# Performance work log

Hardware: AMD Instinct MI355X
Metric: run time of the kernel (lower is better)

The kernel has to match this reference:

```python
import jax, jax.numpy as jnp
import numpy as np

B, N, C = 4, 2048, 768
H = 12
HD = C // H
SCALE = HD ** -0.5


def setup_inputs() -> dict:
    key = jax.random.key(0)
    k1, k2, k3 = jax.random.split(key, 3)
    x = jax.random.normal(k1, (B, N, C), dtype=jnp.float32)
    w_qkv = jax.random.normal(k2, (3 * C, C), dtype=jnp.float32) * (C ** -0.5)
    w_proj = jax.random.normal(k3, (C, C), dtype=jnp.float32) * (C ** -0.5)
    b_proj = jnp.zeros((C,), dtype=jnp.float32)
    return {"x": x, "w_qkv": w_qkv, "w_proj": w_proj, "b_proj": b_proj}


def reference(x, w_qkv, w_proj, b_proj):
    Bx, Nx, Cx = x.shape
    # qkv linear: x @ W^T -> [B, N, 3C], then split into heads
    qkv = jnp.einsum('bnc,dc->bnd', x, w_qkv)
    qkv = qkv.reshape(Bx, Nx, 3, H, HD).transpose(2, 0, 3, 1, 4)  # [3, B, H, N, HD]
    q, k, v = qkv[0], qkv[1], qkv[2]
    attn = jnp.einsum('bhqd,bhkd->bhqk', q, k) * SCALE  # [B, H, N, N]
    attn = jax.nn.softmax(attn, axis=-1)
    out = jnp.einsum('bhqk,bhkd->bhqd', attn, v)  # [B, H, N, HD]
    out = out.transpose(0, 2, 1, 3).reshape(Bx, Nx, Cx)
    out = jnp.einsum('bnc,dc->bnd', out, w_proj) + b_proj
    return out
```

## Files before the change

### kernel.cpp

```cpp
#include <hip/hip_runtime.h>
#include <hip/hip_bf16.h>
#include <stdint.h>

#define DI __device__ __forceinline__

typedef __bf16 bf16x8 __attribute__((ext_vector_type(8)));
typedef float f32x4 __attribute__((ext_vector_type(4)));
typedef unsigned short u16;

DI u16 f2bf(float f) {
  union { float f; uint32_t u; } x; x.f = f;
  uint32_t r = (x.u + 0x7FFFu + ((x.u >> 16) & 1u)) >> 16;
  return (u16)r;
}
DI bf16x8 load16(const u16* p) { return *(const bf16x8*)p; }

DI void async_copy16(void* lds, const void* g) {
  __builtin_amdgcn_global_load_lds(
      (const __attribute__((address_space(1))) uint32_t*)g,
      (__attribute__((address_space(3))) uint32_t*)lds, 16, 0, 0);
}

DI f32x4 mfma16(bf16x8 a, bf16x8 b, f32x4 c) {
  return __builtin_amdgcn_mfma_f32_16x16x32_bf16(a, b, c, 0, 0, 0);
}

DI uint32_t pk_bf16(float a, float b) {
  union { __hip_bfloat162 v; uint32_t u; } r;
  r.v = __float22bfloat162_rn(make_float2(a, b));
  return r.u;
}

#define QSCALE (0.125f * 1.44269504088896340736f)

__global__ __launch_bounds__(256)
void cvt_all(const float* __restrict__ s0, u16* __restrict__ d0, int n0,
             const float* __restrict__ s1, u16* __restrict__ d1, int n1,
             const float* __restrict__ s2, u16* __restrict__ d2, int n2) {
  int i = (blockIdx.x * 256 + threadIdx.x) * 4;
  const float* s; u16* d;
  if (i < n0) { s = s0 + i; d = d0 + i; }
  else if (i < n0 + n1) { s = s1 + (i - n0); d = d1 + (i - n0); }
  else if (i < n0 + n1 + n2) { s = s2 + (i - n0 - n1); d = d2 + (i - n0 - n1); }
  else return;
  float4 v = *(const float4*)s;
  ushort4 o;
  o.x = f2bf(v.x); o.y = f2bf(v.y); o.z = f2bf(v.z); o.w = f2bf(v.w);
  *(ushort4*)d = o;
}

__global__ __launch_bounds__(256)
void gemm_qkv(const u16* __restrict__ A, const u16* __restrict__ Bm,
              u16* __restrict__ Qb, u16* __restrict__ Kb, u16* __restrict__ Vt,
              int M, int N, int K) {
  __shared__ u16 As[128 * 32];
  __shared__ u16 Bs[128 * 32];

  const int tid  = threadIdx.x;
  const int lane = tid & 63;
  const int wave = tid >> 6;
  const int m0 = blockIdx.y * 128;
  const int n0 = blockIdx.x * 128;
  const int wm = (wave & 1) * 64;
  const int wn = (wave >> 1) * 64;
  const int c = lane & 15;
  const int g = lane >> 4;

  f32x4 acc[4][4] = {};

  for (int k0 = 0; k0 < K; k0 += 32) {
#pragma unroll
    for (int i = 0; i < 2; ++i) {
      int j = i * 256 + tid;
      int row = j >> 2;
      int col = (j & 3) * 8;
      async_copy16(&As[j * 8], &A[(size_t)(m0 + row) * K + k0 + col]);
      async_copy16(&Bs[j * 8], &Bm[(size_t)(n0 + row) * K + k0 + col]);
    }
    __syncthreads();

    bf16x8 af[4], bfr[4];
#pragma unroll
    for (int t = 0; t < 4; ++t) {
      af[t]  = *(const bf16x8*)&As[(wm + t * 16 + c) * 32 + g * 8];
      bfr[t] = *(const bf16x8*)&Bs[(wn + t * 16 + c) * 32 + g * 8];
    }
#pragma unroll
    for (int mt = 0; mt < 4; ++mt)
#pragma unroll
      for (int nt = 0; nt < 4; ++nt)
        acc[mt][nt] = mfma16(af[mt], bfr[nt], acc[mt][nt]);
    __syncthreads();
  }

  if (n0 < 768) {
#pragma unroll
    for (int nt = 0; nt < 4; ++nt) {
      int col = n0 + wn + nt * 16 + c;
#pragma unroll
      for (int mt = 0; mt < 4; ++mt)
#pragma unroll
        for (int r = 0; r < 4; ++r) {
          int row = m0 + wm + mt * 16 + g * 4 + r;
          Qb[(size_t)row * 768 + col] = f2bf(acc[mt][nt][r] * QSCALE);
        }
    }
  } else if (n0 < 1536) {
#pragma unroll
    for (int nt = 0; nt < 4; ++nt) {
      int col = n0 - 768 + wn + nt * 16 + c;
#pragma unroll
      for (int mt = 0; mt < 4; ++mt)
#pragma unroll
        for (int r = 0; r < 4; ++r) {
          int row = m0 + wm + mt * 16 + g * 4 + r;
          Kb[(size_t)row * 768 + col] = f2bf(acc[mt][nt][r]);
        }
    }
  } else {
#pragma unroll
    for (int nt = 0; nt < 4; ++nt) {
      int cv = n0 - 1536 + wn + nt * 16 + c;
      int hv = cv >> 6, d = cv & 63;
#pragma unroll
      for (int mt = 0; mt < 4; ++mt) {
        int row = m0 + wm + mt * 16 + g * 4;
        int b = row >> 11, nn = row & 2047;
        ushort4 o;
        o.x = f2bf(acc[mt][nt][0]); o.y = f2bf(acc[mt][nt][1]);
        o.z = f2bf(acc[mt][nt][2]); o.w = f2bf(acc[mt][nt][3]);
        *(ushort4*)&Vt[(((size_t)b * 12 + hv) * 64 + d) * 2048 + nn] = o;
      }
    }
  }
}

__global__ __launch_bounds__(256)
void gemm_proj(const u16* __restrict__ A, const u16* __restrict__ Bm,
               const float* __restrict__ bias, float* __restrict__ Co,
               int M, int N, int K) {
  __shared__ u16 As[128 * 32];
  __shared__ u16 Bs[128 * 32];

  const int tid  = threadIdx.x;
  const int lane = tid & 63;
  const int wave = tid >> 6;
  const int m0 = blockIdx.y * 128;
  const int n0 = blockIdx.x * 128;
  const int wm = (wave & 1) * 64;
  const int wn = (wave >> 1) * 64;
  const int c = lane & 15;
  const int g = lane >> 4;

  f32x4 acc[4][4] = {};

  for (int k0 = 0; k0 < K; k0 += 32) {
#pragma unroll
    for (int i = 0; i < 2; ++i) {
      int j = i * 256 + tid;
      int row = j >> 2;
      int col = (j & 3) * 8;
      async_copy16(&As[j * 8], &A[(size_t)(m0 + row) * K + k0 + col]);
      async_copy16(&Bs[j * 8], &Bm[(size_t)(n0 + row) * K + k0 + col]);
    }
    __syncthreads();

    bf16x8 af[4], bfr[4];
#pragma unroll
    for (int t = 0; t < 4; ++t) {
      af[t]  = *(const bf16x8*)&As[(wm + t * 16 + c) * 32 + g * 8];
      bfr[t] = *(const bf16x8*)&Bs[(wn + t * 16 + c) * 32 + g * 8];
    }
#pragma unroll
    for (int mt = 0; mt < 4; ++mt)
#pragma unroll
      for (int nt = 0; nt < 4; ++nt)
        acc[mt][nt] = mfma16(af[mt], bfr[nt], acc[mt][nt]);
    __syncthreads();
  }

#pragma unroll
  for (int nt = 0; nt < 4; ++nt) {
    int col = n0 + wn + nt * 16 + c;
    float bv = bias[col];
#pragma unroll
    for (int mt = 0; mt < 4; ++mt)
#pragma unroll
      for (int r = 0; r < 4; ++r) {
        int row = m0 + wm + mt * 16 + g * 4 + r;
        Co[(size_t)row * N + col] = acc[mt][nt][r] + bv;
      }
  }
}

__global__ __launch_bounds__(256)
void attn_flash(const u16* __restrict__ Qb, const u16* __restrict__ Kb,
                const u16* __restrict__ Vt, u16* __restrict__ out) {
  __shared__ u16 Ks[2 * 64 * 32];
  __shared__ u16 Vs[2 * 64 * 32];
  __shared__ __align__(16) u16 Plds[4][2 * 16 * 68];

  const int tid  = threadIdx.x;
  const int lane = tid & 63;
  const int wave = tid >> 6;
  const int idx = blockIdx.x;
  const int qchunk = idx & 15;
  const int h = (idx >> 4) % 12;
  const int b = idx / (16 * 12);
  const int q0 = qchunk * 128 + wave * 32;
  const int c = lane & 15;
  const int g = lane >> 4;

  const u16* Qp = Qb + (size_t)b * 2048 * 768 + h * 64;
  const u16* Kp = Kb + (size_t)b * 2048 * 768 + h * 64;
  const u16* Vp = Vt + ((size_t)b * 12 + h) * 64 * 2048;

  u16* pw = &Plds[wave][0];

  bf16x8 qf[2][2];
#pragma unroll
  for (int s = 0; s < 2; ++s) {
    qf[s][0] = load16(&Qp[(size_t)(q0 + s * 16 + c) * 768 + g * 8]);
    qf[s][1] = load16(&Qp[(size_t)(q0 + s * 16 + c) * 768 + 32 + g * 8]);
  }

  bf16x8 ones;
#pragma unroll
  for (int j = 0; j < 8; ++j) ones[j] = (__bf16)1.0f;

  const int j0 = tid, j1 = tid + 256;

  f32x4 o[4][2] = {};
  f32x4 osum[2] = {};

  for (int k0 = 0; k0 < 2048; k0 += 64) {
    {
      int kk0 = (j0 >> 2) & 63, ch0 = j0 & 3;
      int kk1 = (j1 >> 2) & 63, ch1 = j1 & 3;
      async_copy16(&Ks[j0 * 8], &Kp[(size_t)(k0 + kk0) * 768 + ch0 * 8]);
      async_copy16(&Ks[j1 * 8], &Kp[(size_t)(k0 + kk1) * 768 + 32 + ch1 * 8]);
      async_copy16(&Vs[j0 * 8], &Vp[(size_t)kk0 * 2048 + k0 + ch0 * 8]);
      async_copy16(&Vs[j1 * 8], &Vp[(size_t)kk1 * 2048 + k0 + 32 + ch1 * 8]);
    }
    __syncthreads();

#pragma unroll
    for (int kt = 0; kt < 4; ++kt) {
      bf16x8 kf0 = *(const bf16x8*)&Ks[(kt * 16 + c) * 32 + g * 8];
      bf16x8 kf1 = *(const bf16x8*)&Ks[64 * 32 + (kt * 16 + c) * 32 + g * 8];
#pragma unroll
      for (int s = 0; s < 2; ++s) {
        f32x4 z = {};
        f32x4 st = mfma16(kf0, qf[s][0], z);
        st = mfma16(kf1, qf[s][1], st);
        float p0 = __builtin_amdgcn_exp2f(st[0]);
        float p1 = __builtin_amdgcn_exp2f(st[1]);
        float p2 = __builtin_amdgcn_exp2f(st[2]);
        float p3 = __builtin_amdgcn_exp2f(st[3]);
        *(uint2*)&pw[s * 1088 + c * 68 + kt * 16 + g * 4] =
            make_uint2(pk_bf16(p0, p1), pk_bf16(p2, p3));
      }
    }
    __asm__ volatile("s_waitcnt lgkmcnt(0)" ::: "memory");

#pragma unroll
    for (int kt2 = 0; kt2 < 2; ++kt2) {
      bf16x8 pf[2];
#pragma unroll
      for (int s = 0; s < 2; ++s) {
        union { uint2 u2[2]; bf16x8 v; } u;
        u.u2[0] = *(const uint2*)&pw[s * 1088 + c * 68 + kt2 * 32 + g * 8];
        u.u2[1] = *(const uint2*)&pw[s * 1088 + c * 68 + kt2 * 32 + g * 8 + 4];
        pf[s] = u.v;
        osum[s] = mfma16(ones, pf[s], osum[s]);
      }
#pragma unroll
      for (int dt = 0; dt < 4; ++dt) {
        bf16x8 vf = *(const bf16x8*)&Vs[kt2 * 64 * 32 + (dt * 16 + c) * 32 + g * 8];
#pragma unroll
        for (int s = 0; s < 2; ++s)
          o[dt][s] = mfma16(vf, pf[s], o[dt][s]);
      }
    }
    __syncthreads();
  }

#pragma unroll
  for (int s = 0; s < 2; ++s) {
    float inv = 1.f / osum[s][0];
#pragma unroll
    for (int dt = 0; dt < 4; ++dt) {
      uint2 w = make_uint2(pk_bf16(o[dt][s][0] * inv, o[dt][s][1] * inv),
                           pk_bf16(o[dt][s][2] * inv, o[dt][s][3] * inv));
      *(uint2*)&out[(size_t)(b * 2048 + q0 + s * 16 + c) * 768 +
                    h * 64 + dt * 16 + g * 4] = w;
    }
  }
}

extern "C" void kernel_launch(void* const* d_in, const int* in_sizes, int n_in,
                              void* d_out, int out_size, void* d_ws, size_t ws_size,
                              hipStream_t stream) {
  const float* x      = (const float*)d_in[0];
  const float* w_qkv  = (const float*)d_in[1];
  const float* w_proj = (const float*)d_in[2];
  const float* b_proj = (const float*)d_in[3];
  float* out = (float*)d_out;

  const int M = 8192;
  const int C = 768;
  const int NQKV = 2304;

  u16* xb     = (u16*)d_ws;
  u16* wqkvb  = xb + (size_t)M * C;
  u16* wprojb = wqkvb + (size_t)NQKV * C;
  u16* Qb     = wprojb + (size_t)C * C;
  u16* Kb     = Qb + (size_t)M * C;
  u16* Vt     = Kb + (size_t)M * C;
  u16* attn   = Vt + (size_t)M * C;

  dim3 blk(256);
  const int n0 = M * C, n1 = NQKV * C, n2 = C * C;
  cvt_all<<<dim3((n0 + n1 + n2) / 1024), blk, 0, stream>>>(
      x, xb, n0, w_qkv, wqkvb, n1, w_proj, wprojb, n2);

  gemm_qkv<<<dim3(NQKV / 128, M / 128), blk, 0, stream>>>(
      xb, wqkvb, Qb, Kb, Vt, M, NQKV, C);
  attn_flash<<<dim3(4 * 12 * 16), blk, 0, stream>>>(Qb, Kb, Vt, attn);
  gemm_proj<<<dim3(C / 128, M / 128), blk, 0, stream>>>(
      attn, wprojb, b_proj, out, M, C, C);
}
```

Baseline: 237.2 us.

## Double-buffer LDS tiles in all GEMM and attention kernels, vectorize epilogues

Adds double-buffered shared-memory staging to gemm_qkv, gemm_proj and attn_flash, so the next tile's async global-to-LDS copies are issued while the current tile is consumed. This removes one barrier per iteration. The Q/K and proj GEMMs swap MFMA operand order so each lane holds four consecutive columns, which allows packed uint2 and float4 stores instead of scalar stores. gemm_proj also shrinks its M tile to 64 to launch more blocks. The cost is doubled LDS use, which can lower occupancy.

```diff
diff --git a/kernel.cpp b/kernel.cpp
--- a/kernel.cpp
+++ b/kernel.cpp
@@ -53,8 +53,8 @@
 void gemm_qkv(const u16* __restrict__ A, const u16* __restrict__ Bm,
               u16* __restrict__ Qb, u16* __restrict__ Kb, u16* __restrict__ Vt,
               int M, int N, int K) {
-  __shared__ u16 As[128 * 32];
-  __shared__ u16 Bs[128 * 32];
+  __shared__ u16 As[2][128 * 32];
+  __shared__ u16 Bs[2][128 * 32];
 
   const int tid  = threadIdx.x;
   const int lane = tid & 63;
@@ -65,57 +65,75 @@
   const int wn = (wave >> 1) * 64;
   const int c = lane & 15;
   const int g = lane >> 4;
+  const bool qk = (n0 < 1536);
 
   f32x4 acc[4][4] = {};
 
-  for (int k0 = 0; k0 < K; k0 += 32) {
+  auto stage = [&](int buf, int k0) {
 #pragma unroll
     for (int i = 0; i < 2; ++i) {
       int j = i * 256 + tid;
       int row = j >> 2;
       int col = (j & 3) * 8;
-      async_copy16(&As[j * 8], &A[(size_t)(m0 + row) * K + k0 + col]);
-      async_copy16(&Bs[j * 8], &Bm[(size_t)(n0 + row) * K + k0 + col]);
-    }
+      async_copy16(&As[buf][j * 8], &A[(size_t)(m0 + row) * K + k0 + col]);
+      async_copy16(&Bs[buf][j * 8], &Bm[(size_t)(n0 + row) * K + k0 + col]);
+    }
+  };
+
+  stage(0, 0);
+  const int NIT = K / 32;
+  for (int it = 0; it < NIT; ++it) {
+    const int cur = it & 1;
     __syncthreads();
+    if (it + 1 < NIT) stage(1 - cur, (it + 1) * 32);
 
     bf16x8 af[4], bfr[4];
 #pragma unroll
     for (int t = 0; t < 4; ++t) {
-      af[t]  = *(const bf16x8*)&As[(wm + t * 16 + c) * 32 + g * 8];
-      bfr[t] = *(const bf16x8*)&Bs[(wn + t * 16 + c) * 32 + g * 8];
-    }
-#pragma unroll
-    for (int mt = 0; mt < 4; ++mt)
-#pragma unroll
-      for (int nt = 0; nt < 4; ++nt)
-        acc[mt][nt] = mfma16(af[mt], bfr[nt], acc[mt][nt]);
-    __syncthreads();
-  }
-
-  if (n0 < 768) {
-#pragma unroll
-    for (int nt = 0; nt < 4; ++nt) {
-      int col = n0 + wn + nt * 16 + c;
+      af[t]  = *(const bf16x8*)&As[cur][(wm + t * 16 + c) * 32 + g * 8];
+      bfr[t] = *(const bf16x8*)&Bs[cur][(wn + t * 16 + c) * 32 + g * 8];
+    }
+    if (qk) {
 #pragma unroll
       for (int mt = 0; mt < 4; ++mt)
 #pragma unroll
-        for (int r = 0; r < 4; ++r) {
-          int row = m0 + wm + mt * 16 + g * 4 + r;
-          Qb[(size_t)row * 768 + col] = f2bf(acc[mt][nt][r] * QSCALE);
+        for (int nt = 0; nt < 4; ++nt)
+          acc[mt][nt] = mfma16(bfr[nt], af[mt], acc[mt][nt]);
+    } else {
+#pragma unroll
+      for (int mt = 0; mt < 4; ++mt)
+#pragma unroll
+        for (int nt = 0; nt < 4; ++nt)
+          acc[mt][nt] = mfma16(af[mt], bfr[nt], acc[mt][nt]);
+    }
+  }
+
+  if (qk) {
+    if (n0 < 768) {
+#pragma unroll
+      for (int nt = 0; nt < 4; ++nt) {
+        int nb = n0 + wn + nt * 16 + g * 4;
+#pragma unroll
+        for (int mt = 0; mt < 4; ++mt) {
+          int m = m0 + wm + mt * 16 + c;
+          uint2 w = make_uint2(
+              pk_bf16(acc[mt][nt][0] * QSCALE, acc[mt][nt][1] * QSCALE),
+              pk_bf16(acc[mt][nt][2] * QSCALE, acc[mt][nt][3] * QSCALE));
+          *(uint2*)&Qb[(size_t)m * 768 + nb] = w;
         }
-    }
-  } else if (n0 < 1536) {
-#pragma unroll
-    for (int nt = 0; nt < 4; ++nt) {
-      int col = n0 - 768 + wn + nt * 16 + c;
-#pragma unroll
-      for (int mt = 0; mt < 4; ++mt)
-#pragma unroll
-        for (int r = 0; r < 4; ++r) {
-          int row = m0 + wm + mt * 16 + g * 4 + r;
-          Kb[(size_t)row * 768 + col] = f2bf(acc[mt][nt][r]);
+      }
+    } else {
+#pragma unroll
+      for (int nt = 0; nt < 4; ++nt) {
+        int nb = n0 - 768 + wn + nt * 16 + g * 4;
+#pragma unroll
+        for (int mt = 0; mt < 4; ++mt) {
+          int m = m0 + wm + mt * 16 + c;
+          uint2 w = make_uint2(pk_bf16(acc[mt][nt][0], acc[mt][nt][1]),
+                               pk_bf16(acc[mt][nt][2], acc[mt][nt][3]));
+          *(uint2*)&Kb[(size_t)m * 768 + nb] = w;
         }
+      }
     }
   } else {
 #pragma unroll
@@ -139,65 +157,74 @@
 void gemm_proj(const u16* __restrict__ A, const u16* __restrict__ Bm,
                const float* __restrict__ bias, float* __restrict__ Co,
                int M, int N, int K) {
-  __shared__ u16 As[128 * 32];
-  __shared__ u16 Bs[128 * 32];
+  __shared__ u16 As[2][64 * 32];
+  __shared__ u16 Bs[2][128 * 32];
 
   const int tid  = threadIdx.x;
   const int lane = tid & 63;
   const int wave = tid >> 6;
-  const int m0 = blockIdx.y * 128;
+  const int m0 = blockIdx.y * 64;
   const int n0 = blockIdx.x * 128;
-  const int wm = (wave & 1) * 64;
+  const int wm = (wave & 1) * 32;
   const int wn = (wave >> 1) * 64;
   const int c = lane & 15;
   const int g = lane >> 4;
 
-  f32x4 acc[4][4] = {};
-
-  for (int k0 = 0; k0 < K; k0 += 32) {
+  f32x4 acc[2][4] = {};
+
+  auto stage = [&](int buf, int k0) {
+    {
+      int row = tid >> 2, col = (tid & 3) * 8;
+      async_copy16(&As[buf][tid * 8], &A[(size_t)(m0 + row) * K + k0 + col]);
+    }
 #pragma unroll
     for (int i = 0; i < 2; ++i) {
       int j = i * 256 + tid;
-      int row = j >> 2;
-      int col = (j & 3) * 8;
-      async_copy16(&As[j * 8], &A[(size_t)(m0 + row) * K + k0 + col]);
-      async_copy16(&Bs[j * 8], &Bm[(size_t)(n0 + row) * K + k0 + col]);
-    }
+      int row = j >> 2, col = (j & 3) * 8;
+      async_copy16(&Bs[buf][j * 8], &Bm[(size_t)(n0 + row) * K + k0 + col]);
+    }
+  };
+
+  stage(0, 0);
+  const int NIT = K / 32;
+  for (int it = 0; it < NIT; ++it) {
+    const int cur = it & 1;
     __syncthreads();
-
-    bf16x8 af[4], bfr[4];
-#pragma unroll
-    for (int t = 0; t < 4; ++t) {
-      af[t]  = *(const bf16x8*)&As[(wm + t * 16 + c) * 32 + g * 8];
-      bfr[t] = *(const bf16x8*)&Bs[(wn + t * 16 + c) * 32 + g * 8];
-    }
-#pragma unroll
-    for (int mt = 0; mt < 4; ++mt)
+    if (it + 1 < NIT) stage(1 - cur, (it + 1) * 32);
+
+    bf16x8 af[2], bfr[4];
+#pragma unroll
+    for (int t = 0; t < 2; ++t)
+      af[t] = *(const bf16x8*)&As[cur][(wm + t * 16 + c) * 32 + g * 8];
+#pragma unroll
+    for (int t = 0; t < 4; ++t)
+      bfr[t] = *(const bf16x8*)&Bs[cur][(wn + t * 16 + c) * 32 + g * 8];
+#pragma unroll
+    for (int mt = 0; mt < 2; ++mt)
 #pragma unroll
       for (int nt = 0; nt < 4; ++nt)
-        acc[mt][nt] = mfma16(af[mt], bfr[nt], acc[mt][nt]);
-    __syncthreads();
+        acc[mt][nt] = mfma16(bfr[nt], af[mt], acc[mt][nt]);
   }
 
 #pragma unroll
   for (int nt = 0; nt < 4; ++nt) {
-    int col = n0 + wn + nt * 16 + c;
-    float bv = bias[col];
-#pragma unroll
-    for (int mt = 0; mt < 4; ++mt)
-#pragma unroll
-      for (int r = 0; r < 4; ++r) {
-        int row = m0 + wm + mt * 16 + g * 4 + r;
-        Co[(size_t)row * N + col] = acc[mt][nt][r] + bv;
-      }
+    int nb = n0 + wn + nt * 16 + g * 4;
+    float4 bv = *(const float4*)&bias[nb];
+#pragma unroll
+    for (int mt = 0; mt < 2; ++mt) {
+      int m = m0 + wm + mt * 16 + c;
+      float4 w = make_float4(acc[mt][nt][0] + bv.x, acc[mt][nt][1] + bv.y,
+                             acc[mt][nt][2] + bv.z, acc[mt][nt][3] + bv.w);
+      *(float4*)&Co[(size_t)m * N + nb] = w;
+    }
   }
 }
 
 __global__ __launch_bounds__(256)
 void attn_flash(const u16* __restrict__ Qb, const u16* __restrict__ Kb,
                 const u16* __restrict__ Vt, u16* __restrict__ out) {
-  __shared__ u16 Ks[2 * 64 * 32];
-  __shared__ u16 Vs[2 * 64 * 32];
+  __shared__ u16 Ks[2][2 * 64 * 32];
+  __shared__ u16 Vs[2][2 * 64 * 32];
   __shared__ __align__(16) u16 Plds[4][2 * 16 * 68];
 
   const int tid  = threadIdx.x;
@@ -229,25 +256,29 @@
   for (int j = 0; j < 8; ++j) ones[j] = (__bf16)1.0f;
 
   const int j0 = tid, j1 = tid + 256;
+  const int kkA = (j0 >> 2) & 63, chA = j0 & 3;
+  const int kkB = (j1 >> 2) & 63, chB = j1 & 3;
+
+  auto stage = [&](int buf, int k0) {
+    async_copy16(&Ks[buf][j0 * 8], &Kp[(size_t)(k0 + kkA) * 768 + chA * 8]);
+    async_copy16(&Ks[buf][j1 * 8], &Kp[(size_t)(k0 + kkB) * 768 + 32 + chB * 8]);
+    async_copy16(&Vs[buf][j0 * 8], &Vp[(size_t)kkA * 2048 + k0 + chA * 8]);
+    async_copy16(&Vs[buf][j1 * 8], &Vp[(size_t)kkB * 2048 + k0 + 32 + chB * 8]);
+  };
 
   f32x4 o[4][2] = {};
   f32x4 osum[2] = {};
 
-  for (int k0 = 0; k0 < 2048; k0 += 64) {
-    {
-      int kk0 = (j0 >> 2) & 63, ch0 = j0 & 3;
-      int kk1 = (j1 >> 2) & 63, ch1 = j1 & 3;
-      async_copy16(&Ks[j0 * 8], &Kp[(size_t)(k0 + kk0) * 768 + ch0 * 8]);
-      async_copy16(&Ks[j1 * 8], &Kp[(size_t)(k0 + kk1) * 768 + 32 + ch1 * 8]);
-      async_copy16(&Vs[j0 * 8], &Vp[(size_t)kk0 * 2048 + k0 + ch0 * 8]);
-      async_copy16(&Vs[j1 * 8], &Vp[(size_t)kk1 * 2048 + k0 + 32 + ch1 * 8]);
-    }
+  stage(0, 0);
+  for (int i = 0; i < 32; ++i) {
+    const int cur = i & 1;
     __syncthreads();
+    if (i + 1 < 32) stage(1 - cur, (i + 1) * 64);
 
 #pragma unroll
     for (int kt = 0; kt < 4; ++kt) {
-      bf16x8 kf0 = *(const bf16x8*)&Ks[(kt * 16 + c) * 32 + g * 8];
-      bf16x8 kf1 = *(const bf16x8*)&Ks[64 * 32 + (kt * 16 + c) * 32 + g * 8];
+      bf16x8 kf0 = *(const bf16x8*)&Ks[cur][(kt * 16 + c) * 32 + g * 8];
+      bf16x8 kf1 = *(const bf16x8*)&Ks[cur][64 * 32 + (kt * 16 + c) * 32 + g * 8];
 #pragma unroll
       for (int s = 0; s < 2; ++s) {
         f32x4 z = {};
@@ -276,13 +307,12 @@
       }
 #pragma unroll
       for (int dt = 0; dt < 4; ++dt) {
-        bf16x8 vf = *(const bf16x8*)&Vs[kt2 * 64 * 32 + (dt * 16 + c) * 32 + g * 8];
+        bf16x8 vf = *(const bf16x8*)&Vs[cur][kt2 * 64 * 32 + (dt * 16 + c) * 32 + g * 8];
 #pragma unroll
         for (int s = 0; s < 2; ++s)
           o[dt][s] = mfma16(vf, pf[s], o[dt][s]);
       }
     }
-    __syncthreads();
   }
 
 #pragma unroll
@@ -327,6 +357,6 @@
   gemm_qkv<<<dim3(NQKV / 128, M / 128), blk, 0, stream>>>(
       xb, wqkvb, Qb, Kb, Vt, M, NQKV, C);
   attn_flash<<<dim3(4 * 12 * 16), blk, 0, stream>>>(Qb, Kb, Vt, attn);
-  gemm_proj<<<dim3(C / 128, M / 128), blk, 0, stream>>>(
+  gemm_proj<<<dim3(C / 128, M / 64), blk, 0, stream>>>(
       attn, wprojb, b_proj, out, M, C, C);
 }
```

Measured after the change: 259.1 us. 1.09x slower.
